# Kernel tuning notes

Hardware: AMD Instinct MI355X
Metric: run time of the kernel (lower is better)

The kernel has to match this reference:

```python
import jax, jax.numpy as jnp
import numpy as np

B, S, D = 64, 2048, 512


def setup_inputs() -> dict:
    key = jax.random.key(0)
    ks = jax.random.split(key, 7)
    return {
        "c_i_1": jax.random.normal(ks[0], (B, D), dtype=jnp.float32),
        "q": jax.random.normal(ks[1], (B, D), dtype=jnp.float32),
        "cw_s": jax.random.normal(ks[2], (B, S, D), dtype=jnp.float32),
        "W_d2d": jax.random.normal(ks[3], (D, 2 * D), dtype=jnp.float32) * 0.02,
        "b_d": jax.random.normal(ks[4], (D,), dtype=jnp.float32) * 0.02,
        "W_1d": jax.random.normal(ks[5], (1, D), dtype=jnp.float32) * 0.02,
        "b_1": jax.random.normal(ks[6], (1,), dtype=jnp.float32) * 0.02,
    }


def reference(c_i_1, q, cw_s, W_d2d, b_d, W_1d, b_1):
    # concat previous control with question rep: [B, 2D]
    conc_cq = jnp.concatenate([c_i_1, q], axis=1)
    # small GEMM + bias: [B, D]
    cq_i = conc_cq @ W_d2d.T + b_d
    # broadcast multiply against contextual word states: [B, S, D]
    cqcw = cw_s * cq_i[:, None, :]
    # projection to attention logits: [B, S, 1]
    ca_is = jnp.einsum("bsd,od->bso", cqcw, W_1d) + b_1
    # attention over the sequence axis
    cv_is = jax.nn.softmax(ca_is, axis=1)
    # weighted sum -> new control state [B, D]
    c_i = jnp.sum(cv_is * cw_s, axis=1)
    return c_i
```

## Files before the change

kernel.cpp:

```cpp
#include <hip/hip_runtime.h>
#include <math.h>

#define BB 64
#define SS 2048
#define DD 512
#define CH 16
#define ROWS (SS/CH)

__global__ __launch_bounds__(128) void k_w(
    const float* __restrict__ c1, const float* __restrict__ q,
    const float* __restrict__ Wd, const float* __restrict__ bd,
    const float* __restrict__ W1, float* __restrict__ w)
{
    __shared__ float conc[2*DD];
    const int b = blockIdx.y;
    const int t = threadIdx.x;
    for (int i = t; i < DD; i += 128) {
        conc[i]      = c1[b*DD + i];
        conc[DD + i] = q[b*DD + i];
    }
    __syncthreads();
    const int d = blockIdx.x * 128 + t;
    const float4* Wr = (const float4*)(Wd + (size_t)d * (2*DD));
    const float4* cc = (const float4*)conc;
    float acc = 0.f;
    #pragma unroll 8
    for (int k = 0; k < (2*DD)/4; ++k) {
        float4 a = Wr[k];
        float4 c = cc[k];
        acc += a.x*c.x + a.y*c.y + a.z*c.z + a.w*c.w;
    }
    w[b*DD + d] = (acc + bd[d]) * W1[d];
}

__global__ __launch_bounds__(256) void k_pass(
    const float* __restrict__ cw, const float* __restrict__ w,
    float* __restrict__ pm, float* __restrict__ pl, float* __restrict__ pacc)
{
    const int blk  = blockIdx.x;
    const int b    = blk >> 4;
    const int ch   = blk & (CH - 1);
    const int tid  = threadIdx.x;
    const int wave = tid >> 6;
    const int lane = tid & 63;

    const float4* wb = (const float4*)(w + b*DD);
    const float4 w0 = wb[lane];
    const float4 w1 = wb[64 + lane];

    const float* rb = cw + ((size_t)b*SS + (size_t)ch*ROWS + wave) * DD;
    float4 r0 = ((const float4*)rb)[lane];
    float4 r1 = ((const float4*)rb)[64 + lane];

    float m = -INFINITY, l = 0.f;
    float4 a0 = make_float4(0,0,0,0), a1 = make_float4(0,0,0,0);

    #pragma unroll 2
    for (int i = 0; i < ROWS/4; ++i) {
        const int nx = (i < ROWS/4 - 1) ? (i + 1) : i;
        const float4* nb = (const float4*)(rb + (size_t)nx * 4 * DD);
        float4 n0 = nb[lane];
        float4 n1 = nb[64 + lane];

        float dot = r0.x*w0.x + r0.y*w0.y + r0.z*w0.z + r0.w*w0.w
                  + r1.x*w1.x + r1.y*w1.y + r1.z*w1.z + r1.w*w1.w;
        #pragma unroll
        for (int off = 32; off; off >>= 1) dot += __shfl_xor(dot, off, 64);

        if (dot > m) {
            float alpha = __expf(m - dot);
            m = dot;
            l = l*alpha + 1.f;
            a0.x = a0.x*alpha + r0.x; a0.y = a0.y*alpha + r0.y;
            a0.z = a0.z*alpha + r0.z; a0.w = a0.w*alpha + r0.w;
            a1.x = a1.x*alpha + r1.x; a1.y = a1.y*alpha + r1.y;
            a1.z = a1.z*alpha + r1.z; a1.w = a1.w*alpha + r1.w;
        } else {
            float p = __expf(dot - m);
            l += p;
            a0.x += p*r0.x; a0.y += p*r0.y; a0.z += p*r0.z; a0.w += p*r0.w;
            a1.x += p*r1.x; a1.y += p*r1.y; a1.z += p*r1.z; a1.w += p*r1.w;
        }
        r0 = n0; r1 = n1;
    }

    __shared__ float lm[4], ll[4];
    __shared__ float lacc[4][DD];
    if (lane == 0) lm[wave] = m;
    __syncthreads();
    const float M = fmaxf(fmaxf(lm[0], lm[1]), fmaxf(lm[2], lm[3]));
    const float beta = __expf(m - M);
    float4* lw = (float4*)lacc[wave];
    lw[lane]      = make_float4(a0.x*beta, a0.y*beta, a0.z*beta, a0.w*beta);
    lw[64 + lane] = make_float4(a1.x*beta, a1.y*beta, a1.z*beta, a1.w*beta);
    if (lane == 0) ll[wave] = l * beta;
    __syncthreads();
    const float s0 = lacc[0][tid]     + lacc[1][tid]     + lacc[2][tid]     + lacc[3][tid];
    const float s1 = lacc[0][tid+256] + lacc[1][tid+256] + lacc[2][tid+256] + lacc[3][tid+256];
    pacc[(size_t)blk*DD + tid]       = s0;
    pacc[(size_t)blk*DD + tid + 256] = s1;
    if (tid == 0) {
        pm[blk] = M;
        pl[blk] = ll[0] + ll[1] + ll[2] + ll[3];
    }
}

__global__ __launch_bounds__(256) void k_comb(
    const float* __restrict__ pm, const float* __restrict__ pl,
    const float* __restrict__ pacc, float* __restrict__ out)
{
    const int b = blockIdx.x;
    const int tid = threadIdx.x;
    float M = -INFINITY;
    #pragma unroll
    for (int p = 0; p < CH; ++p) M = fmaxf(M, pm[b*CH + p]);
    float L = 0.f, s0 = 0.f, s1 = 0.f;
    #pragma unroll
    for (int p = 0; p < CH; ++p) {
        const float sc = __expf(pm[b*CH + p] - M);
        L  += pl[b*CH + p] * sc;
        s0 += sc * pacc[(size_t)(b*CH + p)*DD + tid];
        s1 += sc * pacc[(size_t)(b*CH + p)*DD + tid + 256];
    }
    out[b*DD + tid]       = s0 / L;
    out[b*DD + tid + 256] = s1 / L;
}

extern "C" void kernel_launch(void* const* d_in, const int* in_sizes, int n_in,
                              void* d_out, int out_size, void* d_ws, size_t ws_size,
                              hipStream_t stream)
{
    const float* c1 = (const float*)d_in[0];
    const float* q  = (const float*)d_in[1];
    const float* cw = (const float*)d_in[2];
    const float* Wd = (const float*)d_in[3];
    const float* bd = (const float*)d_in[4];
    const float* W1 = (const float*)d_in[5];

    float* out  = (float*)d_out;
    float* ws   = (float*)d_ws;
    float* w    = ws;
    float* pm   = w  + BB*DD;
    float* pl   = pm + BB*CH;
    float* pacc = pl + BB*CH;

    k_w   <<<dim3(DD/128, BB), 128, 0, stream>>>(c1, q, Wd, bd, W1, w);
    k_pass<<<BB*CH,            256, 0, stream>>>(cw, w, pm, pl, pacc);
    k_comb<<<BB,               256, 0, stream>>>(pm, pl, pacc, out);
}
```

Baseline: 401.8 us.

## Process four contiguous rows per wave iteration with batched online softmax

Each wave now owns a contiguous block of rows instead of interleaved rows, and handles four rows per iteration. Their dot-product reductions are interleaved and there is one rescale per group. This puts more loads in flight per wave and removes the divergent per-row branch, aiming to hide memory latency on the large streaming read of cw. It raises register use for the double-buffered four-row prefetch, which may lower occupancy. The combine kernel also switches to float2 loads and stores with a single reciprocal.

```diff
diff --git a/kernel.cpp b/kernel.cpp
--- a/kernel.cpp
+++ b/kernel.cpp
@@ -6,6 +6,9 @@
 #define DD 512
 #define CH 16
 #define ROWS (SS/CH)
+#define WROWS (ROWS/4)
+#define RPI 4
+#define ITERS (WROWS/RPI)
 
 __global__ __launch_bounds__(128) void k_w(
     const float* __restrict__ c1, const float* __restrict__ q,
@@ -48,40 +51,63 @@
     const float4 w0 = wb[lane];
     const float4 w1 = wb[64 + lane];
 
-    const float* rb = cw + ((size_t)b*SS + (size_t)ch*ROWS + wave) * DD;
-    float4 r0 = ((const float4*)rb)[lane];
-    float4 r1 = ((const float4*)rb)[64 + lane];
+    const float* rb = cw + ((size_t)b*SS + (size_t)ch*ROWS + (size_t)wave*WROWS) * DD;
+
+    float4 c0[RPI], c1v[RPI];
+    #pragma unroll
+    for (int r = 0; r < RPI; ++r) {
+        const float4* p = (const float4*)(rb + (size_t)r * DD);
+        c0[r]  = p[lane];
+        c1v[r] = p[64 + lane];
+    }
 
     float m = -INFINITY, l = 0.f;
     float4 a0 = make_float4(0,0,0,0), a1 = make_float4(0,0,0,0);
 
     #pragma unroll 2
-    for (int i = 0; i < ROWS/4; ++i) {
-        const int nx = (i < ROWS/4 - 1) ? (i + 1) : i;
-        const float4* nb = (const float4*)(rb + (size_t)nx * 4 * DD);
-        float4 n0 = nb[lane];
-        float4 n1 = nb[64 + lane];
+    for (int i = 0; i < ITERS; ++i) {
+        const int nx = (i + 1 < ITERS) ? (i + 1) : i;
+        const float* nbase = rb + (size_t)nx * RPI * DD;
+        float4 n0[RPI], n1[RPI];
+        #pragma unroll
+        for (int r = 0; r < RPI; ++r) {
+            const float4* p = (const float4*)(nbase + (size_t)r * DD);
+            n0[r] = p[lane];
+            n1[r] = p[64 + lane];
+        }
 
-        float dot = r0.x*w0.x + r0.y*w0.y + r0.z*w0.z + r0.w*w0.w
-                  + r1.x*w1.x + r1.y*w1.y + r1.z*w1.z + r1.w*w1.w;
+        float d_[RPI];
         #pragma unroll
-        for (int off = 32; off; off >>= 1) dot += __shfl_xor(dot, off, 64);
+        for (int r = 0; r < RPI; ++r) {
+            d_[r] = c0[r].x*w0.x + c0[r].y*w0.y + c0[r].z*w0.z + c0[r].w*w0.w
+                  + c1v[r].x*w1.x + c1v[r].y*w1.y + c1v[r].z*w1.z + c1v[r].w*w1.w;
+        }
+        #pragma unroll
+        for (int off = 32; off; off >>= 1) {
+            #pragma unroll
+            for (int r = 0; r < RPI; ++r) d_[r] += __shfl_xor(d_[r], off, 64);
+        }
 
-        if (dot > m) {
-            float alpha = __expf(m - dot);
-            m = dot;
-            l = l*alpha + 1.f;
-            a0.x = a0.x*alpha + r0.x; a0.y = a0.y*alpha + r0.y;
-            a0.z = a0.z*alpha + r0.z; a0.w = a0.w*alpha + r0.w;
-            a1.x = a1.x*alpha + r1.x; a1.y = a1.y*alpha + r1.y;
-            a1.z = a1.z*alpha + r1.z; a1.w = a1.w*alpha + r1.w;
-        } else {
-            float p = __expf(dot - m);
-            l += p;
-            a0.x += p*r0.x; a0.y += p*r0.y; a0.z += p*r0.z; a0.w += p*r0.w;
-            a1.x += p*r1.x; a1.y += p*r1.y; a1.z += p*r1.z; a1.w += p*r1.w;
+        float mn = fmaxf(fmaxf(d_[0], d_[1]), fmaxf(d_[2], d_[3]));
+        mn = fmaxf(mn, m);
+        const float alpha = __expf(m - mn);
+        m = mn;
+        float pr[RPI];
+        #pragma unroll
+        for (int r = 0; r < RPI; ++r) pr[r] = __expf(d_[r] - m);
+        l = l*alpha + (pr[0] + pr[1] + pr[2] + pr[3]);
+        a0.x *= alpha; a0.y *= alpha; a0.z *= alpha; a0.w *= alpha;
+        a1.x *= alpha; a1.y *= alpha; a1.z *= alpha; a1.w *= alpha;
+        #pragma unroll
+        for (int r = 0; r < RPI; ++r) {
+            a0.x += pr[r]*c0[r].x;  a0.y += pr[r]*c0[r].y;
+            a0.z += pr[r]*c0[r].z;  a0.w += pr[r]*c0[r].w;
+            a1.x += pr[r]*c1v[r].x; a1.y += pr[r]*c1v[r].y;
+            a1.z += pr[r]*c1v[r].z; a1.w += pr[r]*c1v[r].w;
         }
-        r0 = n0; r1 = n1;
+
+        #pragma unroll
+        for (int r = 0; r < RPI; ++r) { c0[r] = n0[r]; c1v[r] = n1[r]; }
     }
 
     __shared__ float lm[4], ll[4];
@@ -114,16 +140,18 @@
     float M = -INFINITY;
     #pragma unroll
     for (int p = 0; p < CH; ++p) M = fmaxf(M, pm[b*CH + p]);
-    float L = 0.f, s0 = 0.f, s1 = 0.f;
+    float L = 0.f;
+    float sx = 0.f, sy = 0.f;
     #pragma unroll
     for (int p = 0; p < CH; ++p) {
         const float sc = __expf(pm[b*CH + p] - M);
-        L  += pl[b*CH + p] * sc;
-        s0 += sc * pacc[(size_t)(b*CH + p)*DD + tid];
-        s1 += sc * pacc[(size_t)(b*CH + p)*DD + tid + 256];
+        L += pl[b*CH + p] * sc;
+        const float2 v = ((const float2*)(pacc + (size_t)(b*CH + p)*DD))[tid];
+        sx += sc * v.x;
+        sy += sc * v.y;
     }
-    out[b*DD + tid]       = s0 / L;
-    out[b*DD + tid + 256] = s1 / L;
+    const float inv = 1.f / L;
+    ((float2*)(out + b*DD))[tid] = make_float2(sx*inv, sy*inv);
 }
 
 extern "C" void kernel_launch(void* const* d_in, const int* in_sizes, int n_in,
```

Result: no change. 405.3 us (+0.9%).
